# Performance work log

Measured on AMD Instinct MI355X. Metric: run time of the kernel, lower is better.

Reference implementation:

```python
import jax, jax.numpy as jnp
import numpy as np

N, H, B = 4096, 128, 32
K_MSG, K_INT = 32, 20
CUTOFFS = (3.0, 3.0, 6.0, 6.0, 10.0, 10.0)  # two EGNN layers per backbone
silu = jax.nn.silu


def _lin(key, fi, fo):
    s = 1.0 / np.sqrt(fi)
    return jax.random.uniform(key, (fi, fo), jnp.float32, -s, s)


def setup_inputs():
    ks = jax.random.split(jax.random.key(0), 16)
    L = 6

    def stack(k, fi, fo):
        return jnp.stack([_lin(kk, fi, fo) for kk in jax.random.split(k, L)])

    return dict(
        h=jax.random.normal(ks[0], (N, H), jnp.float32),
        pos=3.0 * jax.random.normal(ks[1], (N, 3), jnp.float32),
        batch=jnp.sort(jax.random.randint(ks[2], (N,), 0, B)),
        edge_w1=stack(ks[3], 2 * H + 1, H), edge_b1=jnp.zeros((L, H)),
        edge_w2=stack(ks[4], H, H), edge_b2=jnp.zeros((L, H)),
        coord_w1=stack(ks[5], H, H), coord_b1=jnp.zeros((L, H)),
        coord_w2=stack(ks[6], H, 1),
        node_w1=stack(ks[7], 2 * H, H), node_b1=jnp.zeros((L, H)),
        node_w2=stack(ks[8], H, H), node_b2=jnp.zeros((L, H)),
        fw1=_lin(ks[9], H, 128), fb1=jnp.zeros((128,)),
        fw2=_lin(ks[10], 128, 3), fb2=jnp.zeros((3,)),
        iw=jnp.stack([_lin(kk, 2 * H + 2, 1) for kk in jax.random.split(ks[11], 3)]),
        ib=jnp.zeros((3, 1)),
        cw1=_lin(ks[12], H, 128), cb1=jnp.zeros((128,)),
        cw2=_lin(ks[13], 128, 64), cb2=jnp.zeros((64,)),
        sw=_lin(ks[14], H, 1), sb=jnp.zeros((1,)),
    )


def _neighbors(pos, batch, cutoff, k):
    # radius graph with fixed fan-out: k nearest same-graph neighbors within cutoff
    p = jax.lax.stop_gradient(pos)
    d2 = jnp.sum((p[:, None, :] - p[None, :, :]) ** 2, -1)  # [N,N]
    valid = (batch[:, None] == batch[None, :]) & (~jnp.eye(p.shape[0], dtype=bool)) & (d2 <= cutoff * cutoff)
    neg, idx = jax.lax.top_k(jnp.where(valid, -d2, -jnp.inf), k)
    return idx, neg > -jnp.inf  # [N,k] int, [N,k] bool validity mask


def _egnn_layer(h, pos, idx, mask, ew1, eb1, ew2, eb2, cw1, cb1, cw2, nw1, nb1, nw2, nb2):
    mf = mask[..., None].astype(h.dtype)  # [N,K,1]
    hj = h[idx]                            # [N,K,H] gather
    rel = pos[:, None, :] - pos[idx]       # [N,K,3]
    d2 = jnp.sum(rel * rel, -1, keepdims=True)
    hi = jnp.broadcast_to(h[:, None, :], hj.shape)
    m = silu(jnp.concatenate([hi, hj, d2], -1) @ ew1 + eb1)
    m = silu(m @ ew2 + eb2) * mf           # masked messages [N,K,H]
    c = silu(m @ cw1 + cb1) @ cw2          # per-edge coord weight [N,K,1]
    cnt = jnp.maximum(jnp.sum(mf, 1), 1.0)
    pos = pos + jnp.sum(rel * c * mf, 1) / cnt
    h = h + (silu(jnp.concatenate([h, jnp.sum(m, 1)], -1) @ nw1 + nb1) @ nw2 + nb2)
    return h, pos


def _forward(h, pos, batch, edge_w1, edge_b1, edge_w2, edge_b2, coord_w1, coord_b1, coord_w2,
             node_w1, node_b1, node_w2, node_b2, fw1, fb1, fw2, fb2, iw, ib, cw1, cb1, cw2, cb2, sw, sb):
    idx = mask = None
    for l in range(6):  # short(3.0) x2, medium(6.0) x2, long(10.0) x2
        if l % 2 == 0:
            idx, mask = _neighbors(pos, batch, CUTOFFS[l], K_MSG)
        h, pos = _egnn_layer(h, pos, idx, mask, edge_w1[l], edge_b1[l], edge_w2[l], edge_b2[l],
                             coord_w1[l], coord_b1[l], coord_w2[l],
                             node_w1[l], node_b1[l], node_w2[l], node_b2[l])
    forces = jnp.tanh(h @ fw1 + fb1) @ fw2 + fb2
    # interaction detection: radius graph (r=10, max 20 neighbors)
    iidx, imask = _neighbors(pos, batch, 10.0, K_INT)
    rel = pos[:, None, :] - pos[iidx]
    dist = jnp.sqrt(jnp.sum(rel * rel, -1, keepdims=True) + 1e-12)  # [N,K,1]
    hi = jnp.broadcast_to(h[:, None, :], (h.shape[0], K_INT, h.shape[1]))
    feats = jnp.concatenate([hi, h[iidx], dist, dist / 10.0], -1)  # [N,K,2H+2]
    scores = jax.nn.sigmoid(jnp.einsum('nkf,tfo->tnko', feats, iw) + ib[:, None, None, :])
    scores = scores * imask[None, :, :, None].astype(h.dtype)  # zero padded edges
    conformer = jax.nn.relu(h @ cw1 + cb1) @ cw2 + cb2
    steric = h @ sw + sb
    return h, pos, forces, scores[0], scores[1], scores[2], conformer, steric


def reference(h, pos, batch, edge_w1, edge_b1, edge_w2, edge_b2, coord_w1, coord_b1, coord_w2,
              node_w1, node_b1, node_w2, node_b2, fw1, fb1, fw2, fb2, iw, ib, cw1, cb1, cw2, cb2, sw, sb):
    return _forward(h, pos, batch, edge_w1, edge_b1, edge_w2, edge_b2, coord_w1, coord_b1, coord_w2,
                    node_w1, node_b1, node_w2, node_b2, fw1, fb1, fw2, fb2, iw, ib, cw1, cb1, cw2, cb2, sw, sb)
```

## Files before the change

### kernel.cpp

```cpp
#include <hip/hip_runtime.h>
#include <hip/hip_bf16.h>

#define NN 4096
#define HD 128
#define KE 32
#define KI 20
#define XLD 132
#define PLOF 68

#define OFF_H   0
#define OFF_POS 524288
#define OFF_F   536576
#define OFF_S   548864
#define OFF_C   794624
#define OFF_ST  1056768

typedef unsigned short u16;
typedef unsigned int u32;
typedef unsigned long long u64;
typedef __attribute__((ext_vector_type(8))) short bf16x8;
typedef __attribute__((ext_vector_type(4))) float f32x4;

__device__ __forceinline__ float b2f(u16 u) {
  union { u32 i; float f; } c; c.i = ((u32)u) << 16; return c.f;
}
__device__ __forceinline__ float silu_f(float x) { return x / (1.f + __expf(-x)); }
__device__ __forceinline__ void stout(void* out, int fp32m, size_t i, float v) {
  if (fp32m) ((float*)out)[i] = v;
  else ((__hip_bfloat16*)out)[i] = __float2bfloat16(v);
}
__device__ __forceinline__ u32 f2b(float f) {
  u32 u = __float_as_uint(f);
  return (u + 0x7fffu + ((u >> 16) & 1u)) >> 16;
}
__device__ __forceinline__ void packplane(float a, float b, u32& H, u32& L) {
  asm("v_cvt_pk_bf16_f32 %0, %1, %2" : "=v"(H) : "v"(a), "v"(b));
  float hfa = __uint_as_float(H << 16);
  float hfb = __uint_as_float(H & 0xffff0000u);
  asm("v_cvt_pk_bf16_f32 %0, %1, %2" : "=v"(L) : "v"(a - hfa), "v"(b - hfb));
}

__global__ void probe_dtype(const u16* __restrict__ h, int* __restrict__ flag) {
  if (threadIdx.x == 0) atomicExch(flag, 0);
  __syncthreads();
  int bad = 0;
  for (int i = threadIdx.x; i < 8192; i += 256) {
    float v = b2f(h[i]);
    if (!(v > -1000.f && v < 1000.f)) bad = 1;
  }
  if (bad) atomicOr(flag, 1);
}

struct CvtTable {
  const void* src[25];
  int dstoff[25];
  int cnt[25];
};

__global__ void convert_all(CvtTable tab, float* __restrict__ wsf, const int* __restrict__ flag) {
  const int seg = blockIdx.y;
  const int i = blockIdx.x * 256 + threadIdx.x;
  if (i >= tab.cnt[seg]) return;
  float v;
  if (*flag) v = ((const float*)tab.src[seg])[i];
  else       v = b2f(((const u16*)tab.src[seg])[i]);
  wsf[tab.dstoff[seg] + i] = v;
}

__global__ void pack_weights(const float* __restrict__ wsf, int offEW1, int offEW2, int offCW1,
                             u16* __restrict__ WBP) {
  int tid = blockIdx.x * 256 + threadIdx.x;
  if (tid >= 18 * 32768) return;
  int m = tid >> 15;
  int rix = tid & 32767;
  int layer = m / 3, s = m % 3;
  const float* src;
  if (s == 0)      src = wsf + offEW1 + (size_t)layer * 257 * HD + 128 * HD;
  else if (s == 1) src = wsf + offEW2 + (size_t)layer * HD * HD;
  else             src = wsf + offCW1 + (size_t)layer * HD * HD;
  int jh = rix & 15, lane = (rix >> 4) & 63, ot = (rix >> 10) & 7, kt = rix >> 13;
  int j = jh & 7;
  int f = kt * 32 + (lane >> 4) * 8 + j;
  int o = ot * 16 + (lane & 15);
  float v = src[f * HD + o];
  u32 hb = f2b(v);
  float hf = __uint_as_float(hb << 16);
  u32 lb = f2b(v - hf);
  WBP[tid] = (jh < 8) ? (u16)hb : (u16)lb;
}

__global__ void graph_bounds(const int* __restrict__ batch, int* __restrict__ gstart) {
  int n = blockIdx.x * 256 + threadIdx.x;
  if (n >= NN) return;
  int v = batch[n];
  int pv = (n == 0) ? -1 : batch[n - 1];
  for (int b = pv + 1; b <= v; b++) gstart[b] = n;
  if (n == NN - 1) for (int b = v + 1; b <= 32; b++) gstart[b] = NN;
}

__global__ __launch_bounds__(256) void neigh_kernel(
    const float* __restrict__ pos, const int* __restrict__ batch,
    const int* __restrict__ gstart, int* __restrict__ idx, int* __restrict__ cnt,
    int Ksel, float cut2) {
  const int lane = threadIdx.x & 63;
  const int i = blockIdx.x * 4 + (threadIdx.x >> 6);
  const int b = batch[i];
  const int gs = gstart[b];
  const int ge = gstart[b + 1];
  const int span = ge - gs;
  const float px = pos[i * 3 + 0], py = pos[i * 3 + 1], pz = pos[i * 3 + 2];
  u64 key[16];
#pragma unroll
  for (int tq = 0; tq < 16; tq++) {
    u64 k64 = ~0ull;
    if (tq * 64 < span) {
      int j = gs + tq * 64 + lane;
      if (j < ge && j != i) {
        float dx = px - pos[j * 3 + 0];
        float dy = py - pos[j * 3 + 1];
        float dz = pz - pos[j * 3 + 2];
        float d2 = dx * dx + dy * dy + dz * dz;
        if (d2 <= cut2) k64 = (((u64)__float_as_uint(d2)) << 32) | (u32)j;
      }
    }
    key[tq] = k64;
  }
  u64 thresh = 0;
  int myidx = i;
  int mycnt = 0;
  for (int s = 0; s < Ksel; s++) {
    u64 m = ~0ull;
#pragma unroll
    for (int tq = 0; tq < 16; tq++) {
      if (tq * 64 < span) {
        u64 kk = key[tq];
        if (kk >= thresh && kk < m) m = kk;
      }
    }
    for (int off = 32; off > 0; off >>= 1) {
      u64 o = __shfl_down(m, (unsigned)off, 64);
      if (o < m) m = o;
    }
    m = __shfl(m, 0, 64);
    if (m != ~0ull) {
      if (lane == s) myidx = (int)(m & 0xffffffffu);
      mycnt++;
      thresh = m + 1;
    } else break;
  }
  if (lane < Ksel) idx[i * Ksel + lane] = myidx;
  if (lane == 0) cnt[i] = mycnt;
}

__global__ __launch_bounds__(256) void hpart_kernel(
    const float* __restrict__ h, const float* __restrict__ ew1,
    const float* __restrict__ eb1, float* __restrict__ hpart) {
  __shared__ float ht[8][HD];
  const int t = threadIdx.x;
  const int n0 = blockIdx.x * 8;
  {
    const int nd = t >> 5, f = (t & 31) * 4;
    *(float4*)(&ht[nd][f]) = *(const float4*)(h + (size_t)(n0 + nd) * HD + f);
  }
  __syncthreads();
  const int nd = t >> 5, ob = (t & 31) * 4;
  float a0 = 0.f, a1 = 0.f, a2 = 0.f, a3 = 0.f;
  float b0 = 0.f, b1 = 0.f, b2 = 0.f, b3 = 0.f;
#pragma unroll 4
  for (int f = 0; f < 64; f++) {
    const float x = ht[nd][f];
    const float4 w4 = *(const float4*)(ew1 + (size_t)f * HD + ob);
    a0 = fmaf(x, w4.x, a0); a1 = fmaf(x, w4.y, a1);
    a2 = fmaf(x, w4.z, a2); a3 = fmaf(x, w4.w, a3);
  }
#pragma unroll 4
  for (int f = 64; f < 128; f++) {
    const float x = ht[nd][f];
    const float4 w4 = *(const float4*)(ew1 + (size_t)f * HD + ob);
    b0 = fmaf(x, w4.x, b0); b1 = fmaf(x, w4.y, b1);
    b2 = fmaf(x, w4.z, b2); b3 = fmaf(x, w4.w, b3);
  }
  const float4 e4 = *(const float4*)(eb1 + ob);
  float4 o4;
  o4.x = a0 + b0 + e4.x; o4.y = a1 + b1 + e4.y;
  o4.z = a2 + b2 + e4.z; o4.w = a3 + b3 + e4.w;
  *(float4*)(hpart + (size_t)(n0 + nd) * HD + ob) = o4;
}

__global__ __launch_bounds__(256) void node_kernel(
    const float* __restrict__ h_in, const float* __restrict__ msum,
    const float* __restrict__ nw1, const float* __restrict__ nb1,
    const float* __restrict__ nw2, const float* __restrict__ nb2,
    float* __restrict__ h_out) {
  __shared__ float ht[8][HD], mt[8][HD], ut[8][HD];
  const int t = threadIdx.x;
  const int n0 = blockIdx.x * 8;
  {
    const int nd = t >> 5, f = (t & 31) * 4;
    *(float4*)(&ht[nd][f]) = *(const float4*)(h_in + (size_t)(n0 + nd) * HD + f);
    *(float4*)(&mt[nd][f]) = *(const float4*)(msum + (size_t)(n0 + nd) * HD + f);
  }
  __syncthreads();
  const int nd = t >> 5, ob = (t & 31) * 4;
  float p1[4] = {0.f, 0.f, 0.f, 0.f}, p2[4] = {0.f, 0.f, 0.f, 0.f};
#pragma unroll 4
  for (int f = 0; f < 128; f++) {
    const float x = ht[nd][f];
    const float4 w4 = *(const float4*)(nw1 + (size_t)f * HD + ob);
    p1[0] = fmaf(x, w4.x, p1[0]); p1[1] = fmaf(x, w4.y, p1[1]);
    p1[2] = fmaf(x, w4.z, p1[2]); p1[3] = fmaf(x, w4.w, p1[3]);
  }
#pragma unroll 4
  for (int f = 0; f < 128; f++) {
    const float x = mt[nd][f];
    const float4 w4 = *(const float4*)(nw1 + (size_t)(128 + f) * HD + ob);
    p2[0] = fmaf(x, w4.x, p2[0]); p2[1] = fmaf(x, w4.y, p2[1]);
    p2[2] = fmaf(x, w4.z, p2[2]); p2[3] = fmaf(x, w4.w, p2[3]);
  }
  {
    const float4 b4 = *(const float4*)(nb1 + ob);
    ut[nd][ob + 0] = silu_f(p1[0] + p2[0] + b4.x);
    ut[nd][ob + 1] = silu_f(p1[1] + p2[1] + b4.y);
    ut[nd][ob + 2] = silu_f(p1[2] + p2[2] + b4.z);
    ut[nd][ob + 3] = silu_f(p1[3] + p2[3] + b4.w);
  }
  __syncthreads();
  float q1[4] = {0.f, 0.f, 0.f, 0.f}, q2[4] = {0.f, 0.f, 0.f, 0.f};
#pragma unroll 4
  for (int f = 0; f < 64; f++) {
    const float x = ut[nd][f];
    const float4 w4 = *(const float4*)(nw2 + (size_t)f * HD + ob);
    q1[0] = fmaf(x, w4.x, q1[0]); q1[1] = fmaf(x, w4.y, q1[1]);
    q1[2] = fmaf(x, w4.z, q1[2]); q1[3] = fmaf(x, w4.w, q1[3]);
  }
#pragma unroll 4
  for (int f = 64; f < 128; f++) {
    const float x = ut[nd][f];
    const float4 w4 = *(const float4*)(nw2 + (size_t)f * HD + ob);
    q2[0] = fmaf(x, w4.x, q2[0]); q2[1] = fmaf(x, w4.y, q2[1]);
    q2[2] = fmaf(x, w4.z, q2[2]); q2[3] = fmaf(x, w4.w, q2[3]);
  }
  {
    const float4 b4 = *(const float4*)(nb2 + ob);
    float4 o4;
    o4.x = ht[nd][ob + 0] + q1[0] + q2[0] + b4.x;
    o4.y = ht[nd][ob + 1] + q1[1] + q2[1] + b4.y;
    o4.z = ht[nd][ob + 2] + q1[2] + q2[2] + b4.z;
    o4.w = ht[nd][ob + 3] + q1[3] + q2[3] + b4.w;
    *(float4*)(h_out + (size_t)(n0 + nd) * HD + ob) = o4;
  }
}

__global__ __launch_bounds__(256, 4) void egnn_edge(
    const float* __restrict__ h_in, const float* __restrict__ pos_in,
    float* __restrict__ pos_out,
    const int* __restrict__ idx, const int* __restrict__ cnt,
    const float* __restrict__ hpart, const float* __restrict__ ew1d2,
    const float* __restrict__ eb2, const float* __restrict__ cb1,
    const float* __restrict__ cw2,
    float* __restrict__ msum, const u16* __restrict__ wbp) {
  __shared__ __align__(16) u32 xp[64 * XLD];
  __shared__ float hp_s[2][HD];
  __shared__ float rel_s[3][64], d2_s[64], mf_s[64], ce_s[64];
  __shared__ float ce_red[64][9];
  __shared__ int idx_s[64], cn_s[2];

  const int t = threadIdx.x;
  const int i0 = blockIdx.x * 2;
  const int lane = t & 63;
  const int w = __builtin_amdgcn_readfirstlane(t >> 6);
  const int l16 = lane & 15, q = lane >> 4;

  if (t < 64) idx_s[t] = idx[(size_t)(i0 + (t >> 5)) * KE + (t & 31)];
  else if (t < 66) cn_s[t - 64] = cnt[i0 + (t - 64)];
  __syncthreads();
  const int nt0 = __builtin_amdgcn_readfirstlane((cn_s[0] + 15) >> 4);
  const int nt1 = __builtin_amdgcn_readfirstlane((cn_s[1] + 15) >> 4);
#define LIVE(Et) (((Et) < 2) ? ((Et) < nt0) : ((Et) - 2 < nt1))

  if (t < 64) {
    const int nd = t >> 5, ic = i0 + nd;
    const int j = idx_s[t];
    const float rx = pos_in[ic * 3 + 0] - pos_in[j * 3 + 0];
    const float ry = pos_in[ic * 3 + 1] - pos_in[j * 3 + 1];
    const float rz = pos_in[ic * 3 + 2] - pos_in[j * 3 + 2];
    rel_s[0][t] = rx; rel_s[1][t] = ry; rel_s[2][t] = rz;
    d2_s[t] = rx * rx + ry * ry + rz * rz;
    mf_s[t] = ((t & 31) < cn_s[nd]) ? 1.0f : 0.0f;
  }
  {
    const int nd = t >> 7, f = t & 127;
    hp_s[nd][f] = hpart[(size_t)(i0 + nd) * HD + f];
  }
  {
    const int e = t & 63;
    const int myEt = e >> 4;
    const bool glive = (myEt < 2) ? (myEt < nt0) : (myEt - 2 < nt1);
    if (glive) {
      const int j = idx_s[e];
      const int f0 = (t >> 6) * 32;
      const float4* src = (const float4*)(h_in + (size_t)j * HD + f0);
#pragma unroll
      for (int half = 0; half < 2; half++) {
        float4 v0 = src[half * 4 + 0], v1 = src[half * 4 + 1];
        float4 v2 = src[half * 4 + 2], v3 = src[half * 4 + 3];
        u32 H0, L0, H1, L1, H2, L2, H3, L3, H4, L4, H5, L5, H6, L6, H7, L7;
        packplane(v0.x, v0.y, H0, L0); packplane(v0.z, v0.w, H1, L1);
        packplane(v1.x, v1.y, H2, L2); packplane(v1.z, v1.w, H3, L3);
        packplane(v2.x, v2.y, H4, L4); packplane(v2.z, v2.w, H5, L5);
        packplane(v3.x, v3.y, H6, L6); packplane(v3.z, v3.w, H7, L7);
        u32* dh = xp + e * XLD + ((f0 + half * 16) >> 1);
        uint4 a; a.x = H0; a.y = H1; a.z = H2; a.w = H3;
        uint4 b; b.x = H4; b.y = H5; b.z = H6; b.w = H7;
        uint4 c; c.x = L0; c.y = L1; c.z = L2; c.w = L3;
        uint4 d; d.x = L4; d.y = L5; d.z = L6; d.w = L7;
        *(uint4*)(dh) = a;        *(uint4*)(dh + 4) = b;
        *(uint4*)(dh + PLOF) = c; *(uint4*)(dh + PLOF + 4) = d;
      }
    }
  }
  __syncthreads();

#define MFMA_PASS(WPBASE, accA, accB)                                          \
  {                                                                            \
    f32x4 z = {0.f, 0.f, 0.f, 0.f};                                            \
    accA[0] = z; accA[1] = z; accA[2] = z; accA[3] = z;                        \
    accB[0] = z; accB[1] = z; accB[2] = z; accB[3] = z;                        \
    bf16x8 whA[4], wlA[4], whB[4], wlB[4];                                     \
    _Pragma("unroll")                                                          \
    for (int kt = 0; kt < 4; kt++) {                                           \
      const u16* wa = (WPBASE) + (size_t)((kt * 8 + w) * 64 + lane) * 16;      \
      whA[kt] = *(const bf16x8*)(wa); wlA[kt] = *(const bf16x8*)(wa + 8);      \
      const u16* wb = (WPBASE) + (size_t)((kt * 8 + w + 4) * 64 + lane) * 16;  \
      whB[kt] = *(const bf16x8*)(wb); wlB[kt] = *(const bf16x8*)(wb + 8);      \
    }                                                                          \
    _Pragma("unroll")                                                          \
    for (int Et = 0; Et < 4; Et++) {                                           \
      if (LIVE(Et)) {                                                          \
        _Pragma("unroll")                                                      \
        for (int kt = 0; kt < 4; kt++) {                                       \
          const u32* xr = xp + (Et * 16 + l16) * XLD + kt * 16 + q * 4;        \
          bf16x8 xh = *(const bf16x8*)(xr);                                    \
          bf16x8 xl = *(const bf16x8*)(xr + PLOF);                             \
          accA[Et] = __builtin_amdgcn_mfma_f32_16x16x32_bf16(whA[kt], xl, accA[Et], 0, 0, 0); \
          accA[Et] = __builtin_amdgcn_mfma_f32_16x16x32_bf16(wlA[kt], xh, accA[Et], 0, 0, 0); \
          accA[Et] = __builtin_amdgcn_mfma_f32_16x16x32_bf16(whA[kt], xh, accA[Et], 0, 0, 0); \
          accB[Et] = __builtin_amdgcn_mfma_f32_16x16x32_bf16(whB[kt], xl, accB[Et], 0, 0, 0); \
          accB[Et] = __builtin_amdgcn_mfma_f32_16x16x32_bf16(wlB[kt], xh, accB[Et], 0, 0, 0); \
          accB[Et] = __builtin_amdgcn_mfma_f32_16x16x32_bf16(whB[kt], xh, accB[Et], 0, 0, 0); \
        }                                                                      \
      }                                                                        \
    }                                                                          \
  }

  {
    f32x4 accA[4], accB[4];
    MFMA_PASS(wbp, accA, accB)
    __syncthreads();
#define EPIB(ACC, OT)                                                          \
    {                                                                          \
      const int o = (OT) * 16 + q * 4;                                         \
      const float4 w24 = *(const float4*)(ew1d2 + o);                          \
      _Pragma("unroll")                                                        \
      for (int Et = 0; Et < 4; Et++) {                                         \
        if (LIVE(Et)) {                                                        \
          const int ee = Et * 16 + l16;                                        \
          const float d2e = d2_s[ee];                                          \
          const float4 hp4 = *(const float4*)(&hp_s[Et >> 1][o]);              \
          float s0 = silu_f(ACC[Et][0] + hp4.x + d2e * w24.x);                 \
          float s1 = silu_f(ACC[Et][1] + hp4.y + d2e * w24.y);                 \
          float s2 = silu_f(ACC[Et][2] + hp4.z + d2e * w24.z);                 \
          float s3 = silu_f(ACC[Et][3] + hp4.w + d2e * w24.w);                 \
          u32 H0, L0, H1, L1;                                                  \
          packplane(s0, s1, H0, L0);                                           \
          packplane(s2, s3, H1, L1);                                           \
          u32* dst = xp + ee * XLD + (OT) * 8 + q * 2;                         \
          uint2 hh; hh.x = H0; hh.y = H1;                                      \
          uint2 ll; ll.x = L0; ll.y = L1;                                      \
          *(uint2*)(dst) = hh;                                                 \
          *(uint2*)(dst + PLOF) = ll;                                          \
        }                                                                      \
      }                                                                        \
    }
    EPIB(accA, w)
    EPIB(accB, (w + 4))
#undef EPIB
  }
  __syncthreads();

  {
    f32x4 accA[4], accB[4];
    MFMA_PASS(wbp + 32768, accA, accB)
    __syncthreads();
    float msA0[4] = {0.f, 0.f, 0.f, 0.f}, msA1[4] = {0.f, 0.f, 0.f, 0.f};
    float msB0[4] = {0.f, 0.f, 0.f, 0.f}, msB1[4] = {0.f, 0.f, 0.f, 0.f};
#define EPIC(ACC, OT, MS0, MS1)                                                \
    {                                                                          \
      const int o = (OT) * 16 + q * 4;                                         \
      const float4 eb4 = *(const float4*)(eb2 + o);                            \
      _Pragma("unroll")                                                        \
      for (int Et = 0; Et < 4; Et++) {                                         \
        if (LIVE(Et)) {                                                        \
          const int ee = Et * 16 + l16;                                        \
          const float mfv = mf_s[ee];                                          \
          float m0 = (mfv != 0.f) ? silu_f(ACC[Et][0] + eb4.x) : 0.f;          \
          float m1 = (mfv != 0.f) ? silu_f(ACC[Et][1] + eb4.y) : 0.f;          \
          float m2 = (mfv != 0.f) ? silu_f(ACC[Et][2] + eb4.z) : 0.f;          \
          float m3 = (mfv != 0.f) ? silu_f(ACC[Et][3] + eb4.w) : 0.f;          \
          if (Et < 2) { MS0[0] += m0; MS0[1] += m1; MS0[2] += m2; MS0[3] += m3; } \
          else        { MS1[0] += m0; MS1[1] += m1; MS1[2] += m2; MS1[3] += m3; } \
          u32 H0, L0, H1, L1;                                                  \
          packplane(m0, m1, H0, L0);                                           \
          packplane(m2, m3, H1, L1);                                           \
          u32* dst = xp + ee * XLD + (OT) * 8 + q * 2;                         \
          uint2 hh; hh.x = H0; hh.y = H1;                                      \
          uint2 ll; ll.x = L0; ll.y = L1;                                      \
          *(uint2*)(dst) = hh;                                                 \
          *(uint2*)(dst + PLOF) = ll;                                          \
        }                                                                      \
      }                                                                        \
    }
    EPIC(accA, w, msA0, msA1)
    EPIC(accB, (w + 4), msB0, msB1)
#undef EPIC
#define RED16(v) v += __shfl_xor(v, 1); v += __shfl_xor(v, 2); \
                 v += __shfl_xor(v, 4); v += __shfl_xor(v, 8);
#pragma unroll
    for (int r = 0; r < 4; r++) { RED16(msA0[r]) RED16(msA1[r]) RED16(msB0[r]) RED16(msB1[r]) }
#undef RED16
    if (l16 == 0) {
      float4 a0; a0.x = msA0[0]; a0.y = msA0[1]; a0.z = msA0[2]; a0.w = msA0[3];
      float4 a1; a1.x = msA1[0]; a1.y = msA1[1]; a1.z = msA1[2]; a1.w = msA1[3];
      float4 b0; b0.x = msB0[0]; b0.y = msB0[1]; b0.z = msB0[2]; b0.w = msB0[3];
      float4 b1; b1.x = msB1[0]; b1.y = msB1[1]; b1.z = msB1[2]; b1.w = msB1[3];
      *(float4*)(msum + (size_t)i0 * HD + w * 16 + q * 4) = a0;
      *(float4*)(msum + (size_t)(i0 + 1) * HD + w * 16 + q * 4) = a1;
      *(float4*)(msum + (size_t)i0 * HD + (w + 4) * 16 + q * 4) = b0;
      *(float4*)(msum + (size_t)(i0 + 1) * HD + (w + 4) * 16 + q * 4) = b1;
    }
  }
  __syncthreads();

  {
    f32x4 accA[4], accB[4];
    MFMA_PASS(wbp + 65536, accA, accB)
#define EPID(ACC, OT)                                                          \
    {                                                                          \
      const int o = (OT) * 16 + q * 4;                                         \
      const float4 cb4 = *(const float4*)(cb1 + o);                            \
      const float4 cw4 = *(const float4*)(cw2 + o);                            \
      _Pragma("unroll")                                                        \
      for (int Et = 0; Et < 4; Et++) {                                         \
        if (LIVE(Et)) {                                                        \
          float p = silu_f(ACC[Et][0] + cb4.x) * cw4.x;                        \
          p = fmaf(silu_f(ACC[Et][1] + cb4.y), cw4.y, p);                      \
          p = fmaf(silu_f(ACC[Et][2] + cb4.z), cw4.z, p);                      \
          p = fmaf(silu_f(ACC[Et][3] + cb4.w), cw4.w, p);                      \
          p += __shfl_xor(p, 16);                                              \
          p += __shfl_xor(p, 32);                                              \
          if (lane < 16) ce_red[Et * 16 + lane][OT] = p;                       \
        }                                                                      \
      }                                                                        \
    }
    EPID(accA, w)
    EPID(accB, (w + 4))
#undef EPID
  }
  __syncthreads();
  if (t < 64) {
    float c = 0.f;
#pragma unroll
    for (int wv = 0; wv < 8; wv++) c += ce_red[t][wv];
    ce_s[t] = (mf_s[t] != 0.f) ? c : 0.f;
  }
  __syncthreads();
  if (t < 6) {
    const int nd = t / 3, ax = t - nd * 3, ic = i0 + nd;
    float s = 0.f;
#pragma unroll
    for (int k = 0; k < 32; k++) s = fmaf(rel_s[ax][nd * 32 + k], ce_s[nd * 32 + k], s);
    const float cntf = fmaxf((float)cn_s[nd], 1.f);
    pos_out[ic * 3 + ax] = pos_in[ic * 3 + ax] + s / cntf;
  }
#undef LIVE
#undef MFMA_PASS
}

__global__ __launch_bounds__(256) void heads_kernel(
    const float* __restrict__ h, const float* __restrict__ pos,
    const float* __restrict__ fw1, const float* __restrict__ fb1,
    const float* __restrict__ fw2, const float* __restrict__ fb2,
    const float* __restrict__ cw1g, const float* __restrict__ cb1g,
    const float* __restrict__ cw2g, const float* __restrict__ cb2g,
    const float* __restrict__ sw, const float* __restrict__ sb,
    const float* __restrict__ iw,
    float* __restrict__ At, float* __restrict__ Bt,
    void* __restrict__ out, const int* __restrict__ flag) {
  __shared__ float hi_s[HD], v1[HD], red_s[256];
  const int i = blockIdx.x, t = threadIdx.x;
  const int fm = *flag;
  if (t < HD) hi_s[t] = h[(size_t)i * HD + t];
  __syncthreads();
  const int o = t & 127, ph = t >> 7;
  {
    float p = 0.f;
#pragma unroll 4
    for (int f = ph * 64; f < ph * 64 + 64; f++) p = fmaf(hi_s[f], fw1[f * HD + o], p);
    red_s[t] = p;
  }
  __syncthreads();
  if (t < HD) v1[t] = tanhf(red_s[t] + red_s[t + 128] + fb1[t]);
  __syncthreads();
  if (t < 3) {
    float p = 0.f;
    for (int f = 0; f < HD; f++) p = fmaf(v1[f], fw2[f * 3 + t], p);
    stout(out, fm, OFF_F + (size_t)i * 3 + t, p + fb2[t]);
  }
  __syncthreads();
  {
    float p = 0.f;
#pragma unroll 4
    for (int f = ph * 64; f < ph * 64 + 64; f++) p = fmaf(hi_s[f], cw1g[f * HD + o], p);
    red_s[t] = p;
  }
  __syncthreads();
  if (t < HD) v1[t] = fmaxf(red_s[t] + red_s[t + 128] + cb1g[t], 0.f);
  __syncthreads();
  {
    const int oo = t & 63, pc = t >> 6;
    float p = 0.f;
#pragma unroll 4
    for (int f = pc * 32; f < pc * 32 + 32; f++) p = fmaf(v1[f], cw2g[f * 64 + oo], p);
    red_s[t] = p;
  }
  __syncthreads();
  if (t < 64)
    stout(out, fm, OFF_C + (size_t)i * 64 + t,
          red_s[t] + red_s[t + 64] + red_s[t + 128] + red_s[t + 192] + cb2g[t]);
  __syncthreads();
  if (t < HD) red_s[t] = hi_s[t] * sw[t];
  __syncthreads();
  if (t == 0) {
    float p = 0.f;
    for (int f = 0; f < HD; f++) p += red_s[f];
    stout(out, fm, OFF_ST + (size_t)i, p + sb[0]);
  }
  __syncthreads();
  {
    const int g = t >> 5, l = t & 31;
    float p = 0.f;
    if (g < 6) {
      const int tt = g >> 1, half = g & 1;
#pragma unroll
      for (int r2 = 0; r2 < 4; r2++)
        p = fmaf(hi_s[l * 4 + r2], iw[tt * 258 + half * 128 + l * 4 + r2], p);
    }
    red_s[t] = p;
  }
  __syncthreads();
  if (t < 6) {
    float p = 0.f;
    for (int l = 0; l < 32; l++) p += red_s[t * 32 + l];
    const int tt = t >> 1;
    if ((t & 1) == 0) At[tt * NN + i] = p;
    else Bt[tt * NN + i] = p;
  }
  if (t < HD) stout(out, fm, OFF_H + (size_t)i * HD + t, hi_s[t]);
  if (t >= 128 && t < 131) stout(out, fm, OFF_POS + (size_t)i * 3 + (t - 128), pos[i * 3 + (t - 128)]);
}

__global__ void scores_kernel(const float* __restrict__ pos, const int* __restrict__ idx2,
                              const int* __restrict__ cnt2, const float* __restrict__ At,
                              const float* __restrict__ Bt, const float* __restrict__ iw,
                              const float* __restrict__ ib, void* __restrict__ out,
                              const int* __restrict__ flag) {
  int tid = blockIdx.x * 256 + threadIdx.x;
  if (tid >= 3 * NN * KI) return;
  const int fm = *flag;
  const int tt = tid / (NN * KI);
  const int r = tid % (NN * KI);
  const int n = r / KI;
  const int k = r % KI;
  float v = 0.f;
  if (k < cnt2[n]) {
    int j = idx2[n * KI + k];
    float dx = pos[n * 3 + 0] - pos[j * 3 + 0];
    float dy = pos[n * 3 + 1] - pos[j * 3 + 1];
    float dz = pos[n * 3 + 2] - pos[j * 3 + 2];
    float d2 = dx * dx + dy * dy + dz * dz;
    float dist = sqrtf(d2 + 1e-12f);
    float s = At[tt * NN + n] + Bt[tt * NN + j] + dist * iw[tt * 258 + 256] +
              (dist * 0.1f) * iw[tt * 258 + 257] + ib[tt];
    v = 1.f / (1.f + __expf(-s));
  }
  stout(out, fm, OFF_S + (size_t)tid, v);
}

extern "C" void kernel_launch(void* const* d_in, const int* in_sizes, int n_in,
                              void* d_out, int out_size, void* d_ws, size_t ws_size,
                              hipStream_t stream) {
  (void)in_sizes; (void)n_in; (void)out_size; (void)ws_size;

  float* wsf = (float*)d_ws;
  float* h_a = wsf + 0;
  float* pos_a = wsf + 524288;
  float* h_b = wsf + 536576;
  float* pos_b = wsf + 1060864;
  float* At = wsf + 1073152;
  float* Bt = wsf + 1085440;
  const int W0 = 1097728;

  static const int wcnt[23] = {197376, 768, 98304, 768, 98304, 768, 768,
                               196608, 768, 98304, 768, 16384, 128, 384, 3,
                               774, 3, 16384, 128, 8192, 64, 128, 1};
  int woff[23];
  {
    int o = W0;
    for (int k = 0; k < 23; k++) { woff[k] = o; o += wcnt[k]; }
  }
  const int IOFF = woff[22] + wcnt[22];
  int* ibase = (int*)d_ws;
  int* idx1 = ibase + IOFF;
  int* cnt1 = idx1 + NN * KE;
  int* idx2 = cnt1 + NN;
  int* cnt2 = idx2 + NN * KI;
  int* gstart = cnt2 + NN;
  int* flag = gstart + 33;
  int wboff = (int)((flag + 1) - ibase);
  wboff = (wboff + 3) & ~3;
  u16* WBP = (u16*)(ibase + wboff);
  float* HPART = wsf + (wboff + 18 * 32768 / 2);
  float* MSUM = HPART + (size_t)NN * HD;

  const float* EW1 = wsf + woff[0];
  const float* EB1 = wsf + woff[1];
  const float* EB2 = wsf + woff[3];
  const float* CB1 = wsf + woff[5];
  const float* CW2 = wsf + woff[6];
  const float* NW1 = wsf + woff[7];
  const float* NB1 = wsf + woff[8];
  const float* NW2 = wsf + woff[9];
  const float* NB2 = wsf + woff[10];
  const float* FW1 = wsf + woff[11];
  const float* FB1 = wsf + woff[12];
  const float* FW2 = wsf + woff[13];
  const float* FB2 = wsf + woff[14];
  const float* IW = wsf + woff[15];
  const float* IB = wsf + woff[16];
  const float* CW1G = wsf + woff[17];
  const float* CB1G = wsf + woff[18];
  const float* CW2G = wsf + woff[19];
  const float* CB2G = wsf + woff[20];
  const float* SW = wsf + woff[21];
  const float* SB = wsf + woff[22];

  probe_dtype<<<1, 256, 0, stream>>>((const u16*)d_in[0], flag);

  CvtTable tab;
  tab.src[0] = d_in[0]; tab.dstoff[0] = 0;       tab.cnt[0] = NN * HD;
  tab.src[1] = d_in[1]; tab.dstoff[1] = 524288;  tab.cnt[1] = NN * 3;
  for (int k = 0; k < 23; k++) {
    tab.src[2 + k] = d_in[3 + k];
    tab.dstoff[2 + k] = woff[k];
    tab.cnt[2 + k] = wcnt[k];
  }
  {
    dim3 g((NN * HD + 255) / 256, 25, 1);
    convert_all<<<g, 256, 0, stream>>>(tab, wsf, flag);
  }
  pack_weights<<<(18 * 32768 + 255) / 256, 256, 0, stream>>>(
      wsf, woff[0], woff[2], woff[4], WBP);

  const int* batch = (const int*)d_in[2];
  graph_bounds<<<NN / 256, 256, 0, stream>>>(batch, gstart);

  const float cut2s[3] = {9.f, 36.f, 100.f};
  float *hin = h_a, *pin = pos_a, *hout = h_b, *pout = pos_b;
  for (int l = 0; l < 6; l++) {
    if ((l & 1) == 0)
      neigh_kernel<<<NN / 4, 256, 0, stream>>>(pin, batch, gstart, idx1, cnt1, KE, cut2s[l >> 1]);
    hpart_kernel<<<NN / 8, 256, 0, stream>>>(hin, EW1 + (size_t)l * 257 * HD,
                                             EB1 + (size_t)l * HD, HPART);
    egnn_edge<<<NN / 2, 256, 0, stream>>>(
        hin, pin, pout, idx1, cnt1, HPART,
        EW1 + (size_t)l * 257 * HD + 256 * HD,
        EB2 + (size_t)l * HD, CB1 + (size_t)l * HD, CW2 + (size_t)l * HD,
        MSUM, WBP + (size_t)l * 3 * 32768);
    node_kernel<<<NN / 8, 256, 0, stream>>>(hin, MSUM,
        NW1 + (size_t)l * 256 * HD, NB1 + (size_t)l * HD,
        NW2 + (size_t)l * HD * HD, NB2 + (size_t)l * HD, hout);
    float* th = hin; hin = hout; hout = th;
    float* tp = pin; pin = pout; pout = tp;
  }
  neigh_kernel<<<NN / 4, 256, 0, stream>>>(pin, batch, gstart, idx2, cnt2, KI, 100.f);
  heads_kernel<<<NN, 256, 0, stream>>>(hin, pin, FW1, FB1, FW2, FB2, CW1G, CB1G, CW2G, CB2G,
                                       SW, SB, IW, At, Bt, d_out, flag);
  scores_kernel<<<(3 * NN * KI + 255) / 256, 256, 0, stream>>>(
      pin, idx2, cnt2, At, Bt, IW, IB, d_out, flag);
}
```

Measured before the change: 899.1 us.

## Fuse hpart, edge and node MLP kernels into one per-layer EGNN kernel

After: 948.1 us. 5.5% more time.

```diff
diff --git a/kernel.cpp b/kernel.cpp
--- a/kernel.cpp
+++ b/kernel.cpp
@@ -152,118 +152,23 @@
   if (lane == 0) cnt[i] = mycnt;
 }
 
-__global__ __launch_bounds__(256) void hpart_kernel(
-    const float* __restrict__ h, const float* __restrict__ ew1,
-    const float* __restrict__ eb1, float* __restrict__ hpart) {
-  __shared__ float ht[8][HD];
-  const int t = threadIdx.x;
-  const int n0 = blockIdx.x * 8;
-  {
-    const int nd = t >> 5, f = (t & 31) * 4;
-    *(float4*)(&ht[nd][f]) = *(const float4*)(h + (size_t)(n0 + nd) * HD + f);
-  }
-  __syncthreads();
-  const int nd = t >> 5, ob = (t & 31) * 4;
-  float a0 = 0.f, a1 = 0.f, a2 = 0.f, a3 = 0.f;
-  float b0 = 0.f, b1 = 0.f, b2 = 0.f, b3 = 0.f;
-#pragma unroll 4
-  for (int f = 0; f < 64; f++) {
-    const float x = ht[nd][f];
-    const float4 w4 = *(const float4*)(ew1 + (size_t)f * HD + ob);
-    a0 = fmaf(x, w4.x, a0); a1 = fmaf(x, w4.y, a1);
-    a2 = fmaf(x, w4.z, a2); a3 = fmaf(x, w4.w, a3);
-  }
-#pragma unroll 4
-  for (int f = 64; f < 128; f++) {
-    const float x = ht[nd][f];
-    const float4 w4 = *(const float4*)(ew1 + (size_t)f * HD + ob);
-    b0 = fmaf(x, w4.x, b0); b1 = fmaf(x, w4.y, b1);
-    b2 = fmaf(x, w4.z, b2); b3 = fmaf(x, w4.w, b3);
-  }
-  const float4 e4 = *(const float4*)(eb1 + ob);
-  float4 o4;
-  o4.x = a0 + b0 + e4.x; o4.y = a1 + b1 + e4.y;
-  o4.z = a2 + b2 + e4.z; o4.w = a3 + b3 + e4.w;
-  *(float4*)(hpart + (size_t)(n0 + nd) * HD + ob) = o4;
-}
-
-__global__ __launch_bounds__(256) void node_kernel(
-    const float* __restrict__ h_in, const float* __restrict__ msum,
+__global__ __launch_bounds__(256, 4) void egnn_layer(
+    const float* __restrict__ h_in, const float* __restrict__ pos_in,
+    float* __restrict__ h_out, float* __restrict__ pos_out,
+    const int* __restrict__ idx, const int* __restrict__ cnt,
+    const float* __restrict__ ew1, const float* __restrict__ eb1,
+    const float* __restrict__ eb2, const float* __restrict__ cb1,
+    const float* __restrict__ cw2,
     const float* __restrict__ nw1, const float* __restrict__ nb1,
     const float* __restrict__ nw2, const float* __restrict__ nb2,
-    float* __restrict__ h_out) {
-  __shared__ float ht[8][HD], mt[8][HD], ut[8][HD];
-  const int t = threadIdx.x;
-  const int n0 = blockIdx.x * 8;
-  {
-    const int nd = t >> 5, f = (t & 31) * 4;
-    *(float4*)(&ht[nd][f]) = *(const float4*)(h_in + (size_t)(n0 + nd) * HD + f);
-    *(float4*)(&mt[nd][f]) = *(const float4*)(msum + (size_t)(n0 + nd) * HD + f);
-  }
-  __syncthreads();
-  const int nd = t >> 5, ob = (t & 31) * 4;
-  float p1[4] = {0.f, 0.f, 0.f, 0.f}, p2[4] = {0.f, 0.f, 0.f, 0.f};
-#pragma unroll 4
-  for (int f = 0; f < 128; f++) {
-    const float x = ht[nd][f];
-    const float4 w4 = *(const float4*)(nw1 + (size_t)f * HD + ob);
-    p1[0] = fmaf(x, w4.x, p1[0]); p1[1] = fmaf(x, w4.y, p1[1]);
-    p1[2] = fmaf(x, w4.z, p1[2]); p1[3] = fmaf(x, w4.w, p1[3]);
-  }
-#pragma unroll 4
-  for (int f = 0; f < 128; f++) {
-    const float x = mt[nd][f];
-    const float4 w4 = *(const float4*)(nw1 + (size_t)(128 + f) * HD + ob);
-    p2[0] = fmaf(x, w4.x, p2[0]); p2[1] = fmaf(x, w4.y, p2[1]);
-    p2[2] = fmaf(x, w4.z, p2[2]); p2[3] = fmaf(x, w4.w, p2[3]);
-  }
-  {
-    const float4 b4 = *(const float4*)(nb1 + ob);
-    ut[nd][ob + 0] = silu_f(p1[0] + p2[0] + b4.x);
-    ut[nd][ob + 1] = silu_f(p1[1] + p2[1] + b4.y);
-    ut[nd][ob + 2] = silu_f(p1[2] + p2[2] + b4.z);
-    ut[nd][ob + 3] = silu_f(p1[3] + p2[3] + b4.w);
-  }
-  __syncthreads();
-  float q1[4] = {0.f, 0.f, 0.f, 0.f}, q2[4] = {0.f, 0.f, 0.f, 0.f};
-#pragma unroll 4
-  for (int f = 0; f < 64; f++) {
-    const float x = ut[nd][f];
-    const float4 w4 = *(const float4*)(nw2 + (size_t)f * HD + ob);
-    q1[0] = fmaf(x, w4.x, q1[0]); q1[1] = fmaf(x, w4.y, q1[1]);
-    q1[2] = fmaf(x, w4.z, q1[2]); q1[3] = fmaf(x, w4.w, q1[3]);
-  }
-#pragma unroll 4
-  for (int f = 64; f < 128; f++) {
-    const float x = ut[nd][f];
-    const float4 w4 = *(const float4*)(nw2 + (size_t)f * HD + ob);
-    q2[0] = fmaf(x, w4.x, q2[0]); q2[1] = fmaf(x, w4.y, q2[1]);
-    q2[2] = fmaf(x, w4.z, q2[2]); q2[3] = fmaf(x, w4.w, q2[3]);
-  }
-  {
-    const float4 b4 = *(const float4*)(nb2 + ob);
-    float4 o4;
-    o4.x = ht[nd][ob + 0] + q1[0] + q2[0] + b4.x;
-    o4.y = ht[nd][ob + 1] + q1[1] + q2[1] + b4.y;
-    o4.z = ht[nd][ob + 2] + q1[2] + q2[2] + b4.z;
-    o4.w = ht[nd][ob + 3] + q1[3] + q2[3] + b4.w;
-    *(float4*)(h_out + (size_t)(n0 + nd) * HD + ob) = o4;
-  }
-}
-
-__global__ __launch_bounds__(256, 4) void egnn_edge(
-    const float* __restrict__ h_in, const float* __restrict__ pos_in,
-    float* __restrict__ pos_out,
-    const int* __restrict__ idx, const int* __restrict__ cnt,
-    const float* __restrict__ hpart, const float* __restrict__ ew1d2,
-    const float* __restrict__ eb2, const float* __restrict__ cb1,
-    const float* __restrict__ cw2,
-    float* __restrict__ msum, const u16* __restrict__ wbp) {
+    const u16* __restrict__ wbp) {
   __shared__ __align__(16) u32 xp[64 * XLD];
-  __shared__ float hp_s[2][HD];
+  __shared__ float hi_s[2][HD], hp_s[2][HD], msum_s[2][HD];
+  __shared__ float shpool[512];
   __shared__ float rel_s[3][64], d2_s[64], mf_s[64], ce_s[64];
-  __shared__ float ce_red[64][9];
   __shared__ int idx_s[64], cn_s[2];
+  float (*ce_red)[8] = reinterpret_cast<float(*)[8]>(shpool);
+  float (*u_s)[HD] = reinterpret_cast<float(*)[HD]>(shpool);
 
   const int t = threadIdx.x;
   const int i0 = blockIdx.x * 2;
@@ -273,6 +178,10 @@
 
   if (t < 64) idx_s[t] = idx[(size_t)(i0 + (t >> 5)) * KE + (t & 31)];
   else if (t < 66) cn_s[t - 64] = cnt[i0 + (t - 64)];
+  {
+    const int nd = t >> 7, f = t & 127;
+    hi_s[nd][f] = h_in[(size_t)(i0 + nd) * HD + f];
+  }
   __syncthreads();
   const int nt0 = __builtin_amdgcn_readfirstlane((cn_s[0] + 15) >> 4);
   const int nt1 = __builtin_amdgcn_readfirstlane((cn_s[1] + 15) >> 4);
@@ -287,10 +196,6 @@
     rel_s[0][t] = rx; rel_s[1][t] = ry; rel_s[2][t] = rz;
     d2_s[t] = rx * rx + ry * ry + rz * rz;
     mf_s[t] = ((t & 31) < cn_s[nd]) ? 1.0f : 0.0f;
-  }
-  {
-    const int nd = t >> 7, f = t & 127;
-    hp_s[nd][f] = hpart[(size_t)(i0 + nd) * HD + f];
   }
   {
     const int e = t & 63;
@@ -318,6 +223,15 @@
         *(uint4*)(dh + PLOF) = c; *(uint4*)(dh + PLOF + 4) = d;
       }
     }
+  }
+  {
+    const int nd = t >> 7, oo = t & 127;
+    float a = 0.f, b = 0.f;
+#pragma unroll 4
+    for (int f = 0; f < 64; f++) a = fmaf(hi_s[nd][f], ew1[(size_t)f * HD + oo], a);
+#pragma unroll 4
+    for (int f = 64; f < 128; f++) b = fmaf(hi_s[nd][f], ew1[(size_t)f * HD + oo], b);
+    hp_s[nd][oo] = a + b + eb1[oo];
   }
   __syncthreads();
 
@@ -360,7 +274,7 @@
 #define EPIB(ACC, OT)                                                          \
     {                                                                          \
       const int o = (OT) * 16 + q * 4;                                         \
-      const float4 w24 = *(const float4*)(ew1d2 + o);                          \
+      const float4 w24 = *(const float4*)(ew1 + 256 * HD + o);                 \
       _Pragma("unroll")                                                        \
       for (int Et = 0; Et < 4; Et++) {                                         \
         if (LIVE(Et)) {                                                        \
@@ -433,10 +347,10 @@
       float4 a1; a1.x = msA1[0]; a1.y = msA1[1]; a1.z = msA1[2]; a1.w = msA1[3];
       float4 b0; b0.x = msB0[0]; b0.y = msB0[1]; b0.z = msB0[2]; b0.w = msB0[3];
       float4 b1; b1.x = msB1[0]; b1.y = msB1[1]; b1.z = msB1[2]; b1.w = msB1[3];
-      *(float4*)(msum + (size_t)i0 * HD + w * 16 + q * 4) = a0;
-      *(float4*)(msum + (size_t)(i0 + 1) * HD + w * 16 + q * 4) = a1;
-      *(float4*)(msum + (size_t)i0 * HD + (w + 4) * 16 + q * 4) = b0;
-      *(float4*)(msum + (size_t)(i0 + 1) * HD + (w + 4) * 16 + q * 4) = b1;
+      *(float4*)(&msum_s[0][w * 16 + q * 4]) = a0;
+      *(float4*)(&msum_s[1][w * 16 + q * 4]) = a1;
+      *(float4*)(&msum_s[0][(w + 4) * 16 + q * 4]) = b0;
+      *(float4*)(&msum_s[1][(w + 4) * 16 + q * 4]) = b1;
     }
   }
   __syncthreads();
@@ -481,6 +395,27 @@
     for (int k = 0; k < 32; k++) s = fmaf(rel_s[ax][nd * 32 + k], ce_s[nd * 32 + k], s);
     const float cntf = fmaxf((float)cn_s[nd], 1.f);
     pos_out[ic * 3 + ax] = pos_in[ic * 3 + ax] + s / cntf;
+  }
+  {
+    const int nd = t >> 7, oo = t & 127;
+    float p1 = 0.f, p2 = 0.f;
+#pragma unroll 4
+    for (int f = 0; f < 128; f++) p1 = fmaf(hi_s[nd][f], nw1[(size_t)f * HD + oo], p1);
+#pragma unroll 4
+    for (int f = 0; f < 128; f++) p2 = fmaf(msum_s[nd][f], nw1[(size_t)(128 + f) * HD + oo], p2);
+    const float uv = silu_f(p1 + p2 + nb1[oo]);
+    __syncthreads();
+    u_s[nd][oo] = uv;
+  }
+  __syncthreads();
+  {
+    const int nd = t >> 7, oo = t & 127;
+    float q1 = 0.f, q2 = 0.f;
+#pragma unroll 4
+    for (int f = 0; f < 64; f++) q1 = fmaf(u_s[nd][f], nw2[(size_t)f * HD + oo], q1);
+#pragma unroll 4
+    for (int f = 64; f < 128; f++) q2 = fmaf(u_s[nd][f], nw2[(size_t)f * HD + oo], q2);
+    h_out[(size_t)(i0 + nd) * HD + oo] = hi_s[nd][oo] + q1 + q2 + nb2[oo];
   }
 #undef LIVE
 #undef MFMA_PASS
@@ -629,8 +564,6 @@
   int wboff = (int)((flag + 1) - ibase);
   wboff = (wboff + 3) & ~3;
   u16* WBP = (u16*)(ibase + wboff);
-  float* HPART = wsf + (wboff + 18 * 32768 / 2);
-  float* MSUM = HPART + (size_t)NN * HD;
 
   const float* EW1 = wsf + woff[0];
   const float* EB1 = wsf + woff[1];
@@ -679,16 +612,13 @@
   for (int l = 0; l < 6; l++) {
     if ((l & 1) == 0)
       neigh_kernel<<<NN / 4, 256, 0, stream>>>(pin, batch, gstart, idx1, cnt1, KE, cut2s[l >> 1]);
-    hpart_kernel<<<NN / 8, 256, 0, stream>>>(hin, EW1 + (size_t)l * 257 * HD,
-                                             EB1 + (size_t)l * HD, HPART);
-    egnn_edge<<<NN / 2, 256, 0, stream>>>(
-        hin, pin, pout, idx1, cnt1, HPART,
-        EW1 + (size_t)l * 257 * HD + 256 * HD,
+    egnn_layer<<<NN / 2, 256, 0, stream>>>(
+        hin, pin, hout, pout, idx1, cnt1,
+        EW1 + (size_t)l * 257 * HD, EB1 + (size_t)l * HD,
         EB2 + (size_t)l * HD, CB1 + (size_t)l * HD, CW2 + (size_t)l * HD,
-        MSUM, WBP + (size_t)l * 3 * 32768);
-    node_kernel<<<NN / 8, 256, 0, stream>>>(hin, MSUM,
         NW1 + (size_t)l * 256 * HD, NB1 + (size_t)l * HD,
-        NW2 + (size_t)l * HD * HD, NB2 + (size_t)l * HD, hout);
+        NW2 + (size_t)l * HD * HD, NB2 + (size_t)l * HD,
+        WBP + (size_t)l * 3 * 32768);
     float* th = hin; hin = hout; hout = th;
     float* tp = pin; pin = pout; pout = tp;
   }
```
